# Performance work log

Hardware: AMD Instinct MI355X
Metric: run time of the kernel (lower is better)

Reference implementation:

```python
import jax, jax.numpy as jnp
import numpy as np

SIZE = 11
SIGMA = 1.5
PAD = 5

def _window2d():
    # cv2.getGaussianKernel(11, 1.5): normalized 1D Gaussian, outer product -> 2D window
    x = np.arange(SIZE) - (SIZE - 1) / 2.0
    g = np.exp(-(x * x) / (2.0 * SIGMA * SIGMA))
    g = g / g.sum()
    return jnp.asarray(np.outer(g, g), dtype=jnp.float32)

def _gconv(x, w):
    # x: [H, W]; replicate ('edge') pad by 5 then valid 11x11 correlation (matches torch
    # Conv2d with padding_mode='replicate'); output [H, W]
    xp = jnp.pad(x, PAD, mode='edge')[None, None]  # [1,1,H+10,W+10]
    y = jax.lax.conv_general_dilated(
        xp, w[None, None], window_strides=(1, 1), padding='VALID',
        dimension_numbers=('NCHW', 'OIHW', 'NCHW'))
    return y[0, 0]

def setup_inputs() -> dict:
    key = jax.random.key(0)
    k1, k2 = jax.random.split(key)
    H = W = 4096
    img1 = jax.random.uniform(k1, (H, W), dtype=jnp.float32) * 255.0
    img2 = jax.random.uniform(k2, (H, W), dtype=jnp.float32) * 255.0
    return {"img1": img1, "img2": img2}

def reference(img1, img2):
    w = _window2d()
    C1 = (0.01 * 255) ** 2
    C2 = (0.03 * 255) ** 2
    mu1 = _gconv(img1, w)
    mu2 = _gconv(img2, w)
    mu1_sq = mu1 * mu1
    mu2_sq = mu2 * mu2
    mu1_mu2 = mu1 * mu2
    sigma1_sq = _gconv(img1 * img1, w) - mu1_sq
    sigma2_sq = _gconv(img2 * img2, w) - mu2_sq
    sigma12 = _gconv(img1 * img2, w) - mu1_mu2
    ssim_map = (2 * mu1_mu2 + C1) * (2 * sigma12 + C2) / (
        (mu1_sq + mu2_sq + C1) * (sigma1_sq + sigma2_sq + C2))
    return jnp.mean(ssim_map)
```

## Files before the change

### kernel.cpp

```cpp
#include <hip/hip_runtime.h>
#include <cmath>

#define IMG_H 4096
#define IMG_W 4096
#define TX 64
#define TY 64
#define HALO 5
#define IN_W (TX + 2*HALO)
#define IN_H (TY + 2*HALO)
#define S_STRIDE (IN_W + 2)
#define SH_STRIDE (TX + 2)

struct GW { float w[11]; };

__global__ __launch_bounds__(256) void ssim_tile_kernel(
    const float* __restrict__ img1, const float* __restrict__ img2,
    float* __restrict__ partial, GW gw) {
  __shared__ float s1[IN_H][S_STRIDE];
  __shared__ float s2[IN_H][S_STRIDE];
  __shared__ float sh[IN_H][SH_STRIDE];

  const int tid  = threadIdx.x;
  const int col0 = blockIdx.x * TX;
  const int row0 = blockIdx.y * TY;

  for (int idx = tid; idx < IN_H * IN_W; idx += 256) {
    int r = idx / IN_W, c = idx - r * IN_W;
    int gr = row0 - HALO + r; gr = gr < 0 ? 0 : (gr > IMG_H - 1 ? IMG_H - 1 : gr);
    int gc = col0 - HALO + c; gc = gc < 0 ? 0 : (gc > IMG_W - 1 ? IMG_W - 1 : gc);
    long off = (long)gr * IMG_W + gc;
    s1[r][c] = img1[off];
    s2[r][c] = img2[off];
  }
  __syncthreads();

  const int cv  = tid & 63;
  const int r0v = (tid >> 6) << 4;

  float res[5][16];

  #pragma unroll
  for (int ch = 0; ch < 5; ++ch) {
    for (int idx = tid; idx < IN_H * 8; idx += 256) {
      int r  = idx >> 3;
      int c0 = (idx & 7) * 8;
      float acc[8];
      #pragma unroll
      for (int i = 0; i < 8; ++i) acc[i] = 0.f;
      #pragma unroll
      for (int k = 0; k < 18; ++k) {
        float a = s1[r][c0 + k];
        float b = s2[r][c0 + k];
        float v = (ch == 0) ? a : (ch == 1) ? b : (ch == 2) ? a * a
                : (ch == 3) ? b * b : a * b;
        #pragma unroll
        for (int i = 0; i < 8; ++i) {
          int kk = k - i;
          if (kk >= 0 && kk < 11) acc[i] = fmaf(gw.w[kk], v, acc[i]);
        }
      }
      #pragma unroll
      for (int i = 0; i < 8; ++i) sh[r][c0 + i] = acc[i];
    }
    __syncthreads();

    {
      float acc[16];
      #pragma unroll
      for (int i = 0; i < 16; ++i) acc[i] = 0.f;
      #pragma unroll
      for (int k = 0; k < 26; ++k) {
        float v = sh[r0v + k][cv];
        #pragma unroll
        for (int i = 0; i < 16; ++i) {
          int kk = k - i;
          if (kk >= 0 && kk < 11) acc[i] = fmaf(gw.w[kk], v, acc[i]);
        }
      }
      #pragma unroll
      for (int i = 0; i < 16; ++i) res[ch][i] = acc[i];
    }
    __syncthreads();
  }

  const float C1 = 6.5025f, C2 = 58.5225f;
  float sum = 0.f;
  #pragma unroll
  for (int i = 0; i < 16; ++i) {
    float mu1 = res[0][i], mu2 = res[1][i];
    float x2  = res[2][i], y2  = res[3][i], xy = res[4][i];
    float mu1s = mu1 * mu1, mu2s = mu2 * mu2, m12 = mu1 * mu2;
    float sg1 = x2 - mu1s, sg2 = y2 - mu2s, sg12 = xy - m12;
    float num = (2.f * m12 + C1) * (2.f * sg12 + C2);
    float den = (mu1s + mu2s + C1) * (sg1 + sg2 + C2);
    sum += num / den;
  }

  #pragma unroll
  for (int off = 32; off > 0; off >>= 1) sum += __shfl_down(sum, off);
  __shared__ float wsum[4];
  int wave = tid >> 6, lane = tid & 63;
  if (lane == 0) wsum[wave] = sum;
  __syncthreads();
  if (tid == 0)
    partial[blockIdx.y * (IMG_W / TX) + blockIdx.x] =
        wsum[0] + wsum[1] + wsum[2] + wsum[3];
}

__global__ __launch_bounds__(256) void ssim_reduce_kernel(
    const float* __restrict__ partial, float* __restrict__ out) {
  const int NBLK = (IMG_H / TY) * (IMG_W / TX);
  int tid = threadIdx.x;
  double s = 0.0;
  for (int i = tid; i < NBLK; i += 256) s += (double)partial[i];
  #pragma unroll
  for (int off = 32; off > 0; off >>= 1) s += __shfl_down(s, off);
  __shared__ double ws[4];
  if ((tid & 63) == 0) ws[tid >> 6] = s;
  __syncthreads();
  if (tid == 0)
    out[0] = (float)((ws[0] + ws[1] + ws[2] + ws[3]) /
                     ((double)IMG_H * (double)IMG_W));
}

extern "C" void kernel_launch(void* const* d_in, const int* in_sizes, int n_in,
                              void* d_out, int out_size, void* d_ws, size_t ws_size,
                              hipStream_t stream) {
  const float* img1 = (const float*)d_in[0];
  const float* img2 = (const float*)d_in[1];
  float* partial = (float*)d_ws;
  float* out = (float*)d_out;

  GW gw;
  double g[11], s = 0.0;
  for (int i = 0; i < 11; ++i) {
    double x = i - 5.0;
    g[i] = exp(-(x * x) / (2.0 * 1.5 * 1.5));
    s += g[i];
  }
  for (int i = 0; i < 11; ++i) gw.w[i] = (float)(g[i] / s);

  dim3 grid(IMG_W / TX, IMG_H / TY);
  ssim_tile_kernel<<<grid, 256, 0, stream>>>(img1, img2, partial, gw);
  ssim_reduce_kernel<<<1, 256, 0, stream>>>(partial, out);
}
```

Baseline: 224.3 us.

## Fuse five SSIM channels into one pass with smaller tiles and vector loads

The tile kernel now computes all five blurred channels (mu1, mu2, x², y², xy) in a single horizontal pass and a single vertical pass. This replaces the five-iteration loop that reloaded shared memory and synchronised twice per channel. Tile height drops from 64 to 16, interior tiles load with float4, the division becomes a hardware reciprocal, and the final reduce uses 1024 threads. The trade-off is a larger halo share (26 input rows per 16 output rows), more partial sums, and slightly lower precision from the approximate reciprocal.

Measured after the change: 248.6 us. +10.8%, slower.

```diff
diff --git a/kernel.cpp b/kernel.cpp
--- a/kernel.cpp
+++ b/kernel.cpp
@@ -4,123 +4,164 @@
 #define IMG_H 4096
 #define IMG_W 4096
 #define TX 64
-#define TY 64
+#define TY 16
 #define HALO 5
-#define IN_W (TX + 2*HALO)
-#define IN_H (TY + 2*HALO)
-#define S_STRIDE (IN_W + 2)
-#define SH_STRIDE (TX + 2)
+#define IN_H 26
+#define SW   84
+#define SHW  68
+#define GRID_X (IMG_W / TX)
+#define GRID_Y (IMG_H / TY)
+#define NPART (GRID_X * GRID_Y)
 
 struct GW { float w[11]; };
 
-__global__ __launch_bounds__(256) void ssim_tile_kernel(
+__device__ __forceinline__ int clampi(int v, int lo, int hi) {
+  return v < lo ? lo : (v > hi ? hi : v);
+}
+
+__global__ __launch_bounds__(256, 3) void ssim_tile_kernel(
     const float* __restrict__ img1, const float* __restrict__ img2,
     float* __restrict__ partial, GW gw) {
-  __shared__ float s1[IN_H][S_STRIDE];
-  __shared__ float s2[IN_H][S_STRIDE];
-  __shared__ float sh[IN_H][SH_STRIDE];
+  __shared__ __align__(16) float s1[IN_H][SW];
+  __shared__ __align__(16) float s2[IN_H][SW];
+  __shared__ __align__(16) float sh[5][IN_H][SHW];
 
   const int tid  = threadIdx.x;
-  const int col0 = blockIdx.x * TX;
-  const int row0 = blockIdx.y * TY;
+  const int bx = blockIdx.x, by = blockIdx.y;
+  const int col0 = bx * TX;
+  const int row0 = by * TY;
 
-  for (int idx = tid; idx < IN_H * IN_W; idx += 256) {
-    int r = idx / IN_W, c = idx - r * IN_W;
-    int gr = row0 - HALO + r; gr = gr < 0 ? 0 : (gr > IMG_H - 1 ? IMG_H - 1 : gr);
-    int gc = col0 - HALO + c; gc = gc < 0 ? 0 : (gc > IMG_W - 1 ? IMG_W - 1 : gc);
-    long off = (long)gr * IMG_W + gc;
-    s1[r][c] = img1[off];
-    s2[r][c] = img2[off];
+  if (bx >= 1 && bx <= GRID_X - 2) {
+    for (int idx = tid; idx < IN_H * 20; idx += 256) {
+      int r = idx / 20, q = idx - r * 20;
+      int gr = clampi(row0 - HALO + r, 0, IMG_H - 1);
+      long base = (long)gr * IMG_W + (col0 - 8 + 4 * q);
+      float4 va = *reinterpret_cast<const float4*>(img1 + base);
+      float4 vb = *reinterpret_cast<const float4*>(img2 + base);
+      *reinterpret_cast<float4*>(&s1[r][4 * q]) = va;
+      *reinterpret_cast<float4*>(&s2[r][4 * q]) = vb;
+    }
+  } else {
+    for (int idx = tid; idx < IN_H * 80; idx += 256) {
+      int r = idx / 80, j = idx - r * 80;
+      int gr = clampi(row0 - HALO + r, 0, IMG_H - 1);
+      int gc = clampi(col0 - 8 + j, 0, IMG_W - 1);
+      long off = (long)gr * IMG_W + gc;
+      s1[r][j] = img1[off];
+      s2[r][j] = img2[off];
+    }
   }
   __syncthreads();
 
-  const int cv  = tid & 63;
-  const int r0v = (tid >> 6) << 4;
-
-  float res[5][16];
-
-  #pragma unroll
-  for (int ch = 0; ch < 5; ++ch) {
-    for (int idx = tid; idx < IN_H * 8; idx += 256) {
-      int r  = idx >> 3;
-      int c0 = (idx & 7) * 8;
-      float acc[8];
+  if (tid < IN_H * 8) {
+    int r = tid >> 3, c0 = (tid & 7) * 8;
+    float a[24], b[24];
+    #pragma unroll
+    for (int m = 0; m < 6; ++m) {
+      float4 va = *reinterpret_cast<const float4*>(&s1[r][c0 + 4 * m]);
+      float4 vb = *reinterpret_cast<const float4*>(&s2[r][c0 + 4 * m]);
+      a[4*m+0] = va.x; a[4*m+1] = va.y; a[4*m+2] = va.z; a[4*m+3] = va.w;
+      b[4*m+0] = vb.x; b[4*m+1] = vb.y; b[4*m+2] = vb.z; b[4*m+3] = vb.w;
+    }
+    float acc[5][8];
+    #pragma unroll
+    for (int ch = 0; ch < 5; ++ch)
       #pragma unroll
-      for (int i = 0; i < 8; ++i) acc[i] = 0.f;
+      for (int i = 0; i < 8; ++i) acc[ch][i] = 0.f;
+    #pragma unroll
+    for (int k = 0; k < 18; ++k) {
+      float va = a[k + 3], vb = b[k + 3];
+      float vaa = va * va, vbb = vb * vb, vab = va * vb;
       #pragma unroll
-      for (int k = 0; k < 18; ++k) {
-        float a = s1[r][c0 + k];
-        float b = s2[r][c0 + k];
-        float v = (ch == 0) ? a : (ch == 1) ? b : (ch == 2) ? a * a
-                : (ch == 3) ? b * b : a * b;
-        #pragma unroll
-        for (int i = 0; i < 8; ++i) {
-          int kk = k - i;
-          if (kk >= 0 && kk < 11) acc[i] = fmaf(gw.w[kk], v, acc[i]);
+      for (int i = 0; i < 8; ++i) {
+        int kk = k - i;
+        if (kk >= 0 && kk < 11) {
+          float w = gw.w[kk];
+          acc[0][i] = fmaf(w, va,  acc[0][i]);
+          acc[1][i] = fmaf(w, vb,  acc[1][i]);
+          acc[2][i] = fmaf(w, vaa, acc[2][i]);
+          acc[3][i] = fmaf(w, vbb, acc[3][i]);
+          acc[4][i] = fmaf(w, vab, acc[4][i]);
         }
       }
-      #pragma unroll
-      for (int i = 0; i < 8; ++i) sh[r][c0 + i] = acc[i];
     }
-    __syncthreads();
+    #pragma unroll
+    for (int ch = 0; ch < 5; ++ch) {
+      *reinterpret_cast<float4*>(&sh[ch][r][c0]) =
+          make_float4(acc[ch][0], acc[ch][1], acc[ch][2], acc[ch][3]);
+      *reinterpret_cast<float4*>(&sh[ch][r][c0 + 4]) =
+          make_float4(acc[ch][4], acc[ch][5], acc[ch][6], acc[ch][7]);
+    }
+  }
+  __syncthreads();
 
-    {
-      float acc[16];
-      #pragma unroll
-      for (int i = 0; i < 16; ++i) acc[i] = 0.f;
-      #pragma unroll
-      for (int k = 0; k < 26; ++k) {
-        float v = sh[r0v + k][cv];
-        #pragma unroll
-        for (int i = 0; i < 16; ++i) {
-          int kk = k - i;
-          if (kk >= 0 && kk < 11) acc[i] = fmaf(gw.w[kk], v, acc[i]);
-        }
+  const int col = tid & 63;
+  const int o0  = (tid >> 6) * 4;
+  float vacc[5][4];
+  #pragma unroll
+  for (int ch = 0; ch < 5; ++ch)
+    #pragma unroll
+    for (int i = 0; i < 4; ++i) vacc[ch][i] = 0.f;
+  #pragma unroll
+  for (int k = 0; k < 14; ++k) {
+    int rr = o0 + k;
+    float v0 = sh[0][rr][col];
+    float v1 = sh[1][rr][col];
+    float v2 = sh[2][rr][col];
+    float v3 = sh[3][rr][col];
+    float v4 = sh[4][rr][col];
+    #pragma unroll
+    for (int i = 0; i < 4; ++i) {
+      int kk = k - i;
+      if (kk >= 0 && kk < 11) {
+        float w = gw.w[kk];
+        vacc[0][i] = fmaf(w, v0, vacc[0][i]);
+        vacc[1][i] = fmaf(w, v1, vacc[1][i]);
+        vacc[2][i] = fmaf(w, v2, vacc[2][i]);
+        vacc[3][i] = fmaf(w, v3, vacc[3][i]);
+        vacc[4][i] = fmaf(w, v4, vacc[4][i]);
       }
-      #pragma unroll
-      for (int i = 0; i < 16; ++i) res[ch][i] = acc[i];
     }
-    __syncthreads();
   }
 
   const float C1 = 6.5025f, C2 = 58.5225f;
   float sum = 0.f;
   #pragma unroll
-  for (int i = 0; i < 16; ++i) {
-    float mu1 = res[0][i], mu2 = res[1][i];
-    float x2  = res[2][i], y2  = res[3][i], xy = res[4][i];
+  for (int i = 0; i < 4; ++i) {
+    float mu1 = vacc[0][i], mu2 = vacc[1][i];
+    float x2  = vacc[2][i], y2 = vacc[3][i], xy = vacc[4][i];
     float mu1s = mu1 * mu1, mu2s = mu2 * mu2, m12 = mu1 * mu2;
     float sg1 = x2 - mu1s, sg2 = y2 - mu2s, sg12 = xy - m12;
     float num = (2.f * m12 + C1) * (2.f * sg12 + C2);
     float den = (mu1s + mu2s + C1) * (sg1 + sg2 + C2);
-    sum += num / den;
+    sum += num * __builtin_amdgcn_rcpf(den);
   }
 
   #pragma unroll
   for (int off = 32; off > 0; off >>= 1) sum += __shfl_down(sum, off);
   __shared__ float wsum[4];
-  int wave = tid >> 6, lane = tid & 63;
-  if (lane == 0) wsum[wave] = sum;
+  if ((tid & 63) == 0) wsum[tid >> 6] = sum;
   __syncthreads();
   if (tid == 0)
-    partial[blockIdx.y * (IMG_W / TX) + blockIdx.x] =
-        wsum[0] + wsum[1] + wsum[2] + wsum[3];
+    partial[by * GRID_X + bx] = wsum[0] + wsum[1] + wsum[2] + wsum[3];
 }
 
-__global__ __launch_bounds__(256) void ssim_reduce_kernel(
+__global__ __launch_bounds__(1024) void ssim_reduce_kernel(
     const float* __restrict__ partial, float* __restrict__ out) {
-  const int NBLK = (IMG_H / TY) * (IMG_W / TX);
   int tid = threadIdx.x;
   double s = 0.0;
-  for (int i = tid; i < NBLK; i += 256) s += (double)partial[i];
+  for (int i = tid; i < NPART; i += 1024) s += (double)partial[i];
   #pragma unroll
   for (int off = 32; off > 0; off >>= 1) s += __shfl_down(s, off);
-  __shared__ double ws[4];
+  __shared__ double ws[16];
   if ((tid & 63) == 0) ws[tid >> 6] = s;
   __syncthreads();
-  if (tid == 0)
-    out[0] = (float)((ws[0] + ws[1] + ws[2] + ws[3]) /
-                     ((double)IMG_H * (double)IMG_W));
+  if (tid == 0) {
+    double t = 0.0;
+    #pragma unroll
+    for (int i = 0; i < 16; ++i) t += ws[i];
+    out[0] = (float)(t / ((double)IMG_H * (double)IMG_W));
+  }
 }
 
 extern "C" void kernel_launch(void* const* d_in, const int* in_sizes, int n_in,
@@ -140,7 +181,7 @@
   }
   for (int i = 0; i < 11; ++i) gw.w[i] = (float)(g[i] / s);
 
-  dim3 grid(IMG_W / TX, IMG_H / TY);
+  dim3 grid(GRID_X, GRID_Y);
   ssim_tile_kernel<<<grid, 256, 0, stream>>>(img1, img2, partial, gw);
-  ssim_reduce_kernel<<<1, 256, 0, stream>>>(partial, out);
+  ssim_reduce_kernel<<<1, 1024, 0, stream>>>(partial, out);
 }
```

## Replace 2D tiled separable convolution with row-streaming register-ring sweep

Applied to the files above, without the earlier changes.

Each block now sweeps 64 output rows over a 512-column strip, streaming one input row at a time through double-buffered shared memory with a prefetch of the next row. Each thread computes horizontal 11-tap sums for two columns and five channels, then scatters them into an 11-slot register ring of vertical accumulators, emitting SSIM terms as rows complete. This removes the per-tile 2D halo staging and the intermediate shared-memory pass, and cuts redundant halo work. In exchange it uses many more registers, launches far fewer blocks, and needs a barrier per row, which may limit latency hiding.

Result: faster. 201.5 us (-10.2%).

```diff
diff --git a/kernel.cpp b/kernel.cpp
--- a/kernel.cpp
+++ b/kernel.cpp
@@ -3,116 +3,167 @@
 
 #define IMG_H 4096
 #define IMG_W 4096
-#define TX 64
-#define TY 64
-#define HALO 5
-#define IN_W (TX + 2*HALO)
-#define IN_H (TY + 2*HALO)
-#define S_STRIDE (IN_W + 2)
-#define SH_STRIDE (TX + 2)
+#define GX 8
+#define GY 64
+#define TCOLS 512
+#define R 64
+#define NITER (R + 10)
+#define SWORDS 528
+#define NF4 132
+#define NSLOT (2*NF4)
 
 struct GW { float w[11]; };
 
-__global__ __launch_bounds__(256) void ssim_tile_kernel(
+__device__ __forceinline__ int clampi(int v, int lo, int hi) {
+  return v < lo ? lo : (v > hi ? hi : v);
+}
+
+__global__ __launch_bounds__(256, 2) void ssim_sweep_kernel(
     const float* __restrict__ img1, const float* __restrict__ img2,
     float* __restrict__ partial, GW gw) {
-  __shared__ float s1[IN_H][S_STRIDE];
-  __shared__ float s2[IN_H][S_STRIDE];
-  __shared__ float sh[IN_H][SH_STRIDE];
+  __shared__ __align__(16) float sbuf[2][2][SWORDS];
 
   const int tid  = threadIdx.x;
-  const int col0 = blockIdx.x * TX;
-  const int row0 = blockIdx.y * TY;
+  const int bx = blockIdx.x, by = blockIdx.y;
+  const int c0   = bx * TCOLS;
+  const int row0 = by * R;
+  const bool edge = (bx == 0) || (bx == GX - 1);
 
-  for (int idx = tid; idx < IN_H * IN_W; idx += 256) {
-    int r = idx / IN_W, c = idx - r * IN_W;
-    int gr = row0 - HALO + r; gr = gr < 0 ? 0 : (gr > IMG_H - 1 ? IMG_H - 1 : gr);
-    int gc = col0 - HALO + c; gc = gc < 0 ? 0 : (gc > IMG_W - 1 ? IMG_W - 1 : gc);
-    long off = (long)gr * IMG_W + gc;
-    s1[r][c] = img1[off];
-    s2[r][c] = img2[off];
+  const int  j0   = tid;
+  const bool has2 = (tid < NSLOT - 256);
+  const int  j1   = tid + 256;
+
+  auto load_slot = [&](int j, int gr) -> float4 {
+    const float* img = (j < NF4) ? img1 : img2;
+    int wo = ((j < NF4) ? j : j - NF4) * 4;
+    long rowbase = (long)gr * IMG_W;
+    int gc = c0 - 8 + wo;
+    if (!edge) {
+      return *reinterpret_cast<const float4*>(img + rowbase + gc);
+    } else {
+      float4 v;
+      v.x = img[rowbase + clampi(gc + 0, 0, IMG_W - 1)];
+      v.y = img[rowbase + clampi(gc + 1, 0, IMG_W - 1)];
+      v.z = img[rowbase + clampi(gc + 2, 0, IMG_W - 1)];
+      v.w = img[rowbase + clampi(gc + 3, 0, IMG_W - 1)];
+      return v;
+    }
+  };
+  auto store_slot = [&](int buf, int j, float4 v) {
+    int im = (j < NF4) ? 0 : 1;
+    int wo = ((j < NF4) ? j : j - NF4) * 4;
+    *reinterpret_cast<float4*>(&sbuf[buf][im][wo]) = v;
+  };
+
+  {
+    int gr = clampi(row0 - 5, 0, IMG_H - 1);
+    float4 v0 = load_slot(j0, gr);
+    store_slot(0, j0, v0);
+    if (has2) { float4 v1 = load_slot(j1, gr); store_slot(0, j1, v1); }
   }
-  __syncthreads();
 
-  const int cv  = tid & 63;
-  const int r0v = (tid >> 6) << 4;
+  float acc[5][11][2];
+  #pragma unroll
+  for (int ch = 0; ch < 5; ++ch)
+    #pragma unroll
+    for (int s = 0; s < 11; ++s) { acc[ch][s][0] = 0.f; acc[ch][s][1] = 0.f; }
 
-  float res[5][16];
+  float sum = 0.f;
+  const int base = 2 * tid + 2;
 
-  #pragma unroll
-  for (int ch = 0; ch < 5; ++ch) {
-    for (int idx = tid; idx < IN_H * 8; idx += 256) {
-      int r  = idx >> 3;
-      int c0 = (idx & 7) * 8;
-      float acc[8];
-      #pragma unroll
-      for (int i = 0; i < 8; ++i) acc[i] = 0.f;
-      #pragma unroll
-      for (int k = 0; k < 18; ++k) {
-        float a = s1[r][c0 + k];
-        float b = s2[r][c0 + k];
-        float v = (ch == 0) ? a : (ch == 1) ? b : (ch == 2) ? a * a
-                : (ch == 3) ? b * b : a * b;
+  for (int g = 0; g < 7; ++g) {
+    #pragma unroll
+    for (int p = 0; p < 11; ++p) {
+      const int i = g * 11 + p;
+      if (i < NITER) {
+        __syncthreads();
+
+        float4 pre0, pre1;
+        const bool pf = (i + 1 < NITER);
+        if (pf) {
+          int gr = clampi(row0 - 5 + i + 1, 0, IMG_H - 1);
+          pre0 = load_slot(j0, gr);
+          if (has2) pre1 = load_slot(j1, gr);
+        }
+
+        const int cur = i & 1;
+        float wa[14], wb[14];
         #pragma unroll
-        for (int i = 0; i < 8; ++i) {
-          int kk = k - i;
-          if (kk >= 0 && kk < 11) acc[i] = fmaf(gw.w[kk], v, acc[i]);
+        for (int m = 0; m < 7; ++m) {
+          float2 fa = *reinterpret_cast<const float2*>(&sbuf[cur][0][base + 2 * m]);
+          float2 fb = *reinterpret_cast<const float2*>(&sbuf[cur][1][base + 2 * m]);
+          wa[2 * m] = fa.x; wa[2 * m + 1] = fa.y;
+          wb[2 * m] = fb.x; wb[2 * m + 1] = fb.y;
+        }
+
+        {
+          const int rs = (p + 5) % 11;
+          #pragma unroll
+          for (int ch = 0; ch < 5; ++ch) { acc[ch][rs][0] = 0.f; acc[ch][rs][1] = 0.f; }
+        }
+
+        float h[5][2];
+        #pragma unroll
+        for (int ch = 0; ch < 5; ++ch) { h[ch][0] = 0.f; h[ch][1] = 0.f; }
+        #pragma unroll
+        for (int j = 0; j < 11; ++j) {
+          const float wj = gw.w[j];
+          float a1 = wa[j + 1], a2 = wa[j + 2];
+          float b1 = wb[j + 1], b2 = wb[j + 2];
+          h[0][0] = fmaf(wj, a1, h[0][0]);      h[0][1] = fmaf(wj, a2, h[0][1]);
+          h[1][0] = fmaf(wj, b1, h[1][0]);      h[1][1] = fmaf(wj, b2, h[1][1]);
+          h[2][0] = fmaf(wj, a1 * a1, h[2][0]); h[2][1] = fmaf(wj, a2 * a2, h[2][1]);
+          h[3][0] = fmaf(wj, b1 * b1, h[3][0]); h[3][1] = fmaf(wj, b2 * b2, h[3][1]);
+          h[4][0] = fmaf(wj, a1 * b1, h[4][0]); h[4][1] = fmaf(wj, a2 * b2, h[4][1]);
+        }
+
+        #pragma unroll
+        for (int d = -5; d <= 5; ++d) {
+          const int s = (p + d + 11) % 11;
+          const float wd = gw.w[5 - d];
+          #pragma unroll
+          for (int ch = 0; ch < 5; ++ch) {
+            acc[ch][s][0] = fmaf(wd, h[ch][0], acc[ch][s][0]);
+            acc[ch][s][1] = fmaf(wd, h[ch][1], acc[ch][s][1]);
+          }
+        }
+
+        if (i >= 10) {
+          const int cs = (p + 6) % 11;
+          const float C1 = 6.5025f, C2 = 58.5225f;
+          #pragma unroll
+          for (int x = 0; x < 2; ++x) {
+            float mu1 = acc[0][cs][x], mu2 = acc[1][cs][x];
+            float x2 = acc[2][cs][x], y2 = acc[3][cs][x], xy = acc[4][cs][x];
+            float mu1s = mu1 * mu1, mu2s = mu2 * mu2, m12 = mu1 * mu2;
+            float num = (2.f * m12 + C1) * (2.f * (xy - m12) + C2);
+            float den = (mu1s + mu2s + C1) * ((x2 - mu1s) + (y2 - mu2s) + C2);
+            sum += num * __builtin_amdgcn_rcpf(den);
+          }
+        }
+
+        if (pf) {
+          store_slot((i + 1) & 1, j0, pre0);
+          if (has2) store_slot((i + 1) & 1, j1, pre1);
         }
       }
-      #pragma unroll
-      for (int i = 0; i < 8; ++i) sh[r][c0 + i] = acc[i];
     }
-    __syncthreads();
-
-    {
-      float acc[16];
-      #pragma unroll
-      for (int i = 0; i < 16; ++i) acc[i] = 0.f;
-      #pragma unroll
-      for (int k = 0; k < 26; ++k) {
-        float v = sh[r0v + k][cv];
-        #pragma unroll
-        for (int i = 0; i < 16; ++i) {
-          int kk = k - i;
-          if (kk >= 0 && kk < 11) acc[i] = fmaf(gw.w[kk], v, acc[i]);
-        }
-      }
-      #pragma unroll
-      for (int i = 0; i < 16; ++i) res[ch][i] = acc[i];
-    }
-    __syncthreads();
-  }
-
-  const float C1 = 6.5025f, C2 = 58.5225f;
-  float sum = 0.f;
-  #pragma unroll
-  for (int i = 0; i < 16; ++i) {
-    float mu1 = res[0][i], mu2 = res[1][i];
-    float x2  = res[2][i], y2  = res[3][i], xy = res[4][i];
-    float mu1s = mu1 * mu1, mu2s = mu2 * mu2, m12 = mu1 * mu2;
-    float sg1 = x2 - mu1s, sg2 = y2 - mu2s, sg12 = xy - m12;
-    float num = (2.f * m12 + C1) * (2.f * sg12 + C2);
-    float den = (mu1s + mu2s + C1) * (sg1 + sg2 + C2);
-    sum += num / den;
   }
 
   #pragma unroll
   for (int off = 32; off > 0; off >>= 1) sum += __shfl_down(sum, off);
   __shared__ float wsum[4];
-  int wave = tid >> 6, lane = tid & 63;
-  if (lane == 0) wsum[wave] = sum;
+  if ((tid & 63) == 0) wsum[tid >> 6] = sum;
   __syncthreads();
   if (tid == 0)
-    partial[blockIdx.y * (IMG_W / TX) + blockIdx.x] =
-        wsum[0] + wsum[1] + wsum[2] + wsum[3];
+    partial[by * GX + bx] = wsum[0] + wsum[1] + wsum[2] + wsum[3];
 }
 
 __global__ __launch_bounds__(256) void ssim_reduce_kernel(
     const float* __restrict__ partial, float* __restrict__ out) {
-  const int NBLK = (IMG_H / TY) * (IMG_W / TX);
+  const int NPART = GX * GY;
   int tid = threadIdx.x;
-  double s = 0.0;
-  for (int i = tid; i < NBLK; i += 256) s += (double)partial[i];
+  double s = (double)partial[tid] + (double)partial[tid + 256];
   #pragma unroll
   for (int off = 32; off > 0; off >>= 1) s += __shfl_down(s, off);
   __shared__ double ws[4];
@@ -121,6 +172,7 @@
   if (tid == 0)
     out[0] = (float)((ws[0] + ws[1] + ws[2] + ws[3]) /
                      ((double)IMG_H * (double)IMG_W));
+  (void)NPART;
 }
 
 extern "C" void kernel_launch(void* const* d_in, const int* in_sizes, int n_in,
@@ -140,7 +192,7 @@
   }
   for (int i = 0; i < 11; ++i) gw.w[i] = (float)(g[i] / s);
 
-  dim3 grid(IMG_W / TX, IMG_H / TY);
-  ssim_tile_kernel<<<grid, 256, 0, stream>>>(img1, img2, partial, gw);
+  dim3 grid(GX, GY);
+  ssim_sweep_kernel<<<grid, 256, 0, stream>>>(img1, img2, partial, gw);
   ssim_reduce_kernel<<<1, 256, 0, stream>>>(partial, out);
 }
```
